# Performance work log

Measured on AMD Instinct MI355X. Metric: run time of the kernel, lower is better.

## Reference

```python
import jax, jax.numpy as jnp
import numpy as np

SCALE = 0.02

def setup_inputs() -> dict:
    key = jax.random.key(0)
    k1, k2 = jax.random.split(key)
    B, D, T, H = 2, 1024, 2048, 16
    x = jax.random.normal(k1, (B, D, T), dtype=jnp.float32)
    qkv = jax.random.normal(k2, (3, H, D, D // H), dtype=jnp.float32) * SCALE
    return {"x": x, "qkv": qkv}

def reference(x, qkv):
    B, D, T = x.shape
    H = qkv.shape[1]
    # fused QKV projection: (B,D,T) x (3,H,D,Dh) -> (3,B,H,T,Dh)
    proj = jnp.einsum('bdt,nhdD->nbhtD', x, qkv)
    q, k, v = proj[0], proj[1], proj[2]
    scale = jnp.sqrt(jnp.asarray(D // H, dtype=x.dtype))
    # scores: (B,H,T,T)
    attn = jax.nn.softmax(jnp.einsum('bhtD,bhTD->bhtT', q, k) / scale, axis=-1)
    # weighted values, head dim placed before time: (B,H,Dh,T)
    out = jnp.einsum('bhtT,bhTD->bhDt', attn, v)
    return out.reshape(B, D, T)
```

## Files before the change

### kernel.cpp

```cpp
#include <hip/hip_runtime.h>

#define B_ 2
#define D_ 1024
#define T_ 2048
#define H_ 16
#define DH_ 64
#define BH_ (B_ * H_)

typedef __attribute__((ext_vector_type(8))) short bf16x8;
typedef __attribute__((ext_vector_type(8))) unsigned short u16x8;
typedef __attribute__((ext_vector_type(4))) float f32x4;

__device__ __forceinline__ unsigned short f2bf(float f) {
    unsigned u = __float_as_uint(f);
    u += 0x7fffu + ((u >> 16) & 1u);
    return (unsigned short)(u >> 16);
}

__global__ __launch_bounds__(256) void xpose_kernel(
    const float* __restrict__ x, unsigned short* __restrict__ xT)
{
    __shared__ __align__(16) unsigned short Ls[64][68];
    const int t0 = blockIdx.x * 64;
    const int d0 = blockIdx.y * 64;
    const int b  = blockIdx.z;
    const int tid = threadIdx.x;

    const float* xb = x + (size_t)b * D_ * T_ + (size_t)d0 * T_ + t0;
    #pragma unroll
    for (int p = 0; p < 4; p++) {
        int i4  = tid + p * 256;
        int row = i4 >> 4;
        int c4  = (i4 & 15) << 2;
        float4 v = *(const float4*)(xb + (size_t)row * T_ + c4);
        ushort4 u;
        u.x = f2bf(v.x); u.y = f2bf(v.y); u.z = f2bf(v.z); u.w = f2bf(v.w);
        *(ushort4*)&Ls[row][c4] = u;
    }
    __syncthreads();
    unsigned short* ob = xT + (size_t)b * T_ * D_ + (size_t)t0 * D_ + d0;
    #pragma unroll
    for (int p = 0; p < 2; p++) {
        int i    = tid + p * 256;
        int orow = i >> 3;
        int oc8  = (i & 7) * 8;
        u16x8 tv;
        #pragma unroll
        for (int j = 0; j < 8; j++) tv[j] = Ls[oc8 + j][orow];
        *(u16x8*)(ob + (size_t)orow * D_ + oc8) = tv;
    }
}

__global__ __launch_bounds__(256) void wpose_kernel(
    const float* __restrict__ w, unsigned short* __restrict__ wT)
{
    __shared__ __align__(16) unsigned short Ls[64][68];
    const int d0 = blockIdx.x * 64;
    const int nh = blockIdx.y;
    const int tid = threadIdx.x;

    const float* wb = w + (size_t)nh * D_ * DH_ + (size_t)d0 * DH_;
    #pragma unroll
    for (int p = 0; p < 4; p++) {
        int i4  = tid + p * 256;
        int row = i4 >> 4;
        int c4  = (i4 & 15) << 2;
        float4 v = *(const float4*)(wb + (size_t)row * DH_ + c4);
        ushort4 u;
        u.x = f2bf(v.x); u.y = f2bf(v.y); u.z = f2bf(v.z); u.w = f2bf(v.w);
        *(ushort4*)&Ls[row][c4] = u;
    }
    __syncthreads();
    unsigned short* ob = wT + (size_t)nh * DH_ * D_ + d0;
    #pragma unroll
    for (int p = 0; p < 2; p++) {
        int i    = tid + p * 256;
        int orow = i >> 3;
        int oc8  = (i & 7) * 8;
        u16x8 tv;
        #pragma unroll
        for (int j = 0; j < 8; j++) tv[j] = Ls[oc8 + j][orow];
        *(u16x8*)(ob + (size_t)orow * D_ + oc8) = tv;
    }
}

#define LX 72

__global__ __launch_bounds__(256) void proj_mfma_kernel(
    const unsigned short* __restrict__ xT, const unsigned short* __restrict__ wT,
    unsigned short* __restrict__ qk, unsigned short* __restrict__ vT)
{
    __shared__ __align__(16) unsigned short Buf[18432];
    unsigned short* Xs = Buf;
    unsigned short* Ws = Buf + 9216;
    unsigned short* Es = Buf;

    const int t0 = blockIdx.x * 128;
    const int y  = blockIdx.y;
    const int n  = y >> 4;
    const int b  = (y >> 3) & 1;
    const int hp = y & 7;

    const unsigned short* xb = xT + (size_t)b * T_ * D_ + (size_t)t0 * D_;
    const unsigned short* wb = wT + (size_t)(n * 16 + 2 * hp) * DH_ * D_;

    const int tid  = threadIdx.x;
    const int wv   = tid >> 6;
    const int lane = tid & 63;
    const int c15  = lane & 15;
    const int quad = lane >> 4;
    const int tq   = (wv & 1) * 64;
    const int dq   = (wv >> 1) * 64;

    f32x4 acc[4][4];
    #pragma unroll
    for (int mt = 0; mt < 4; mt++)
        #pragma unroll
        for (int nt = 0; nt < 4; nt++)
            acc[mt][nt] = (f32x4){0.f, 0.f, 0.f, 0.f};

    for (int k0 = 0; k0 < D_; k0 += 64) {
        __syncthreads();
        #pragma unroll
        for (int p = 0; p < 4; p++) {
            int i    = tid + p * 256;
            int row  = i >> 3;
            int col8 = (i & 7) * 8;
            *(u16x8*)&Xs[row * LX + col8] =
                *(const u16x8*)(xb + (size_t)row * D_ + k0 + col8);
            *(u16x8*)&Ws[row * LX + col8] =
                *(const u16x8*)(wb + (size_t)row * D_ + k0 + col8);
        }
        __syncthreads();

        bf16x8 af[4][2], bf[4][2];
        #pragma unroll
        for (int mt = 0; mt < 4; mt++)
            #pragma unroll
            for (int s = 0; s < 2; s++)
                af[mt][s] = *(bf16x8*)&Xs[(tq + mt * 16 + c15) * LX + quad * 8 + s * 32];
        #pragma unroll
        for (int nt = 0; nt < 4; nt++)
            #pragma unroll
            for (int s = 0; s < 2; s++)
                bf[nt][s] = *(bf16x8*)&Ws[(dq + nt * 16 + c15) * LX + quad * 8 + s * 32];

        #pragma unroll
        for (int mt = 0; mt < 4; mt++)
            #pragma unroll
            for (int nt = 0; nt < 4; nt++)
                #pragma unroll
                for (int s = 0; s < 2; s++)
                    acc[mt][nt] = __builtin_amdgcn_mfma_f32_16x16x32_bf16(
                        af[mt][s], bf[nt][s], acc[mt][nt], 0, 0, 0);
    }

    const float scale = (n == 0) ? 0.125f : 1.0f;
    __syncthreads();
    #pragma unroll
    for (int mt = 0; mt < 4; mt++)
        #pragma unroll
        for (int nt = 0; nt < 4; nt++)
            #pragma unroll
            for (int r = 0; r < 4; r++)
                Es[(tq + mt * 16 + quad * 4 + r) * 136 + dq + nt * 16 + c15] =
                    f2bf(acc[mt][nt][r] * scale);
    __syncthreads();

    if (n < 2) {
        #pragma unroll
        for (int p = 0; p < 8; p++) {
            int i    = tid + p * 256;
            int row  = i >> 4;
            int col8 = (i & 15) * 8;
            int head = col8 >> 6;
            unsigned short* ob = qk +
                ((size_t)(n * 32 + b * 16 + 2 * hp + head) * T_ + t0 + row) * DH_ + (col8 & 63);
            *(u16x8*)ob = *(u16x8*)&Es[row * 136 + col8];
        }
    } else {
        #pragma unroll
        for (int p = 0; p < 8; p++) {
            int i    = tid + p * 256;
            int orow = i >> 4;
            int oc8  = (i & 15) * 8;
            int head = orow >> 6;
            u16x8 tv;
            #pragma unroll
            for (int j = 0; j < 8; j++) tv[j] = Es[(oc8 + j) * 136 + orow];
            unsigned short* ob = vT +
                (size_t)(b * 16 + 2 * hp + head) * DH_ * T_ +
                (size_t)(orow & 63) * T_ + t0 + oc8;
            *(u16x8*)ob = tv;
        }
    }
}

#define LQ 72

__global__ __launch_bounds__(256) void attn_mfma_kernel(
    const unsigned short* __restrict__ qk, const unsigned short* __restrict__ vT,
    float* __restrict__ out)
{
    __shared__ __align__(16) unsigned char smem[37376];
    unsigned short* Ks  = (unsigned short*)smem;
    unsigned short* Vs  = (unsigned short*)(smem + 9216);
    unsigned short* Psb = (unsigned short*)(smem + 18432);
    float*          Os  = (float*)smem;
    float*          Lrow = (float*)(smem + 36864);

    const int t0 = blockIdx.x * 128;
    const int bh = blockIdx.y;

    const unsigned short* qg = qk + ((size_t)bh * T_ + t0) * DH_;
    const unsigned short* kg = qk + ((size_t)(BH_ + bh) * T_) * DH_;
    const unsigned short* vg = vT + (size_t)bh * DH_ * T_;

    const int tid  = threadIdx.x;
    const int wv   = tid >> 6;
    const int lane = tid & 63;
    const int c15  = lane & 15;
    const int quad = lane >> 4;

    unsigned short* Ps = Psb + wv * 2304;

    bf16x8 bq[2][2];
    #pragma unroll
    for (int g = 0; g < 2; g++)
        #pragma unroll
        for (int s = 0; s < 2; s++)
            bq[g][s] = *(const bf16x8*)(qg +
                (size_t)(wv * 32 + g * 16 + c15) * DH_ + quad * 8 + s * 32);

    float lsum[2] = {0.f, 0.f};
    f32x4 Oacc[2][4];
    #pragma unroll
    for (int g = 0; g < 2; g++)
        #pragma unroll
        for (int nt = 0; nt < 4; nt++)
            Oacc[g][nt] = (f32x4){0.f, 0.f, 0.f, 0.f};

    for (int tau = 0; tau < T_; tau += 64) {
        __syncthreads();
        #pragma unroll
        for (int p = 0; p < 2; p++) {
            int i    = tid + p * 256;
            int row  = i >> 3;
            int col8 = (i & 7) * 8;
            *(u16x8*)&Ks[row * LQ + col8] =
                *(const u16x8*)(kg + (size_t)(tau + row) * DH_ + col8);
            *(u16x8*)&Vs[row * LQ + col8] =
                *(const u16x8*)(vg + (size_t)row * T_ + tau + col8);
        }
        __syncthreads();

        bf16x8 ak[4][2];
        #pragma unroll
        for (int mt = 0; mt < 4; mt++)
            #pragma unroll
            for (int s = 0; s < 2; s++)
                ak[mt][s] = *(bf16x8*)&Ks[(mt * 16 + c15) * LQ + quad * 8 + s * 32];

        #pragma unroll
        for (int g = 0; g < 2; g++) {
            #pragma unroll
            for (int mt = 0; mt < 4; mt++) {
                f32x4 sa = (f32x4){0.f, 0.f, 0.f, 0.f};
                #pragma unroll
                for (int s = 0; s < 2; s++)
                    sa = __builtin_amdgcn_mfma_f32_16x16x32_bf16(ak[mt][s], bq[g][s], sa, 0, 0, 0);
                float p0 = __expf(sa[0]);
                float p1 = __expf(sa[1]);
                float p2 = __expf(sa[2]);
                float p3 = __expf(sa[3]);
                lsum[g] += (p0 + p1) + (p2 + p3);
                uint2 pk;
                pk.x = (unsigned)f2bf(p0) | ((unsigned)f2bf(p1) << 16);
                pk.y = (unsigned)f2bf(p2) | ((unsigned)f2bf(p3) << 16);
                *(uint2*)&Ps[(g * 16 + c15) * LQ + mt * 16 + quad * 4] = pk;
            }
        }
        __syncthreads();

        bf16x8 bv[4][2];
        #pragma unroll
        for (int nt = 0; nt < 4; nt++)
            #pragma unroll
            for (int s = 0; s < 2; s++)
                bv[nt][s] = *(bf16x8*)&Vs[(nt * 16 + c15) * LQ + quad * 8 + s * 32];
        #pragma unroll
        for (int g = 0; g < 2; g++)
            #pragma unroll
            for (int s = 0; s < 2; s++) {
                bf16x8 ap = *(bf16x8*)&Ps[(g * 16 + c15) * LQ + quad * 8 + s * 32];
                #pragma unroll
                for (int nt = 0; nt < 4; nt++)
                    Oacc[g][nt] = __builtin_amdgcn_mfma_f32_16x16x32_bf16(
                        ap, bv[nt][s], Oacc[g][nt], 0, 0, 0);
            }
    }

    #pragma unroll
    for (int g = 0; g < 2; g++) {
        lsum[g] += __shfl_xor(lsum[g], 16);
        lsum[g] += __shfl_xor(lsum[g], 32);
    }
    if (lane < 16) {
        Lrow[wv * 32 + lane]      = lsum[0];
        Lrow[wv * 32 + 16 + lane] = lsum[1];
    }
    __syncthreads();

    #pragma unroll
    for (int g = 0; g < 2; g++) {
        float linv[4];
        #pragma unroll
        for (int r = 0; r < 4; r++)
            linv[r] = 1.0f / Lrow[wv * 32 + g * 16 + quad * 4 + r];
        #pragma unroll
        for (int nt = 0; nt < 4; nt++)
            #pragma unroll
            for (int r = 0; r < 4; r++)
                Os[(nt * 16 + c15) * 132 + wv * 32 + g * 16 + quad * 4 + r] =
                    Oacc[g][nt][r] * linv[r];
    }
    __syncthreads();

    const int b = bh >> 4, h = bh & 15;
    float* og = out + (size_t)b * D_ * T_ + (size_t)(h * DH_) * T_ + t0;
    #pragma unroll
    for (int p = 0; p < 8; p++) {
        int i   = tid + p * 256;
        int row = i >> 5;
        int c4  = (i & 31) << 2;
        *(float4*)(og + (size_t)row * T_ + c4) = *(float4*)&Os[row * 132 + c4];
    }
}

extern "C" void kernel_launch(void* const* d_in, const int* in_sizes, int n_in,
                              void* d_out, int out_size, void* d_ws, size_t ws_size,
                              hipStream_t stream)
{
    const float* x = (const float*)d_in[0];
    const float* w = (const float*)d_in[1];
    float* out = (float*)d_out;

    unsigned short* qk = (unsigned short*)d_ws;
    unsigned short* vT = (unsigned short*)((char*)d_ws + (24u << 20));
    unsigned short* xT = (unsigned short*)((char*)d_ws + (32u << 20));
    unsigned short* wT = (unsigned short*)((char*)d_ws + (40u << 20));

    xpose_kernel<<<dim3(T_ / 64, D_ / 64, B_), 256, 0, stream>>>(x, xT);
    wpose_kernel<<<dim3(D_ / 64, 3 * H_), 256, 0, stream>>>(w, wT);
    proj_mfma_kernel<<<dim3(T_ / 128, 48), 256, 0, stream>>>(xT, wT, qk, vT);
    attn_mfma_kernel<<<dim3(T_ / 128, BH_), 256, 0, stream>>>(qk, vT, out);
}
```

Before: 203.6 us.

## Make attention waves independent, reading K/V from global memory with XCD-aware block mapping

The attention kernel now gives each wave 16 query rows (64 per block) and has every wave read K and V fragments straight from global memory. This drops the shared-memory K/V staging and the block-wide barriers. Block indices are remapped so the blocks sharing a batch-head land on the same XCD, which should improve L2 reuse of K/V. The trade is more global/L2 traffic and less reuse per block, since each wave reloads the full K/V, and the grid doubles to 1024 blocks.

```diff
diff --git a/kernel.cpp b/kernel.cpp
--- a/kernel.cpp
+++ b/kernel.cpp
@@ -202,15 +202,13 @@
     const unsigned short* __restrict__ qk, const unsigned short* __restrict__ vT,
     float* __restrict__ out)
 {
-    __shared__ __align__(16) unsigned char smem[37376];
-    unsigned short* Ks  = (unsigned short*)smem;
-    unsigned short* Vs  = (unsigned short*)(smem + 9216);
-    unsigned short* Psb = (unsigned short*)(smem + 18432);
-    float*          Os  = (float*)smem;
-    float*          Lrow = (float*)(smem + 36864);
-
-    const int t0 = blockIdx.x * 128;
-    const int bh = blockIdx.y;
+    __shared__ __align__(16) unsigned short Sm[10240];
+
+    const int flat = blockIdx.y * 32 + blockIdx.x;
+    const int xcd  = flat & 7;
+    const int slot = flat >> 3;
+    const int bh   = xcd * 4 + (slot >> 5);
+    const int t0   = (slot & 31) * 64;
 
     const unsigned short* qg = qk + ((size_t)bh * T_ + t0) * DH_;
     const unsigned short* kg = qk + ((size_t)(BH_ + bh) * T_) * DH_;
@@ -222,118 +220,74 @@
     const int c15  = lane & 15;
     const int quad = lane >> 4;
 
-    unsigned short* Ps = Psb + wv * 2304;
-
-    bf16x8 bq[2][2];
-    #pragma unroll
-    for (int g = 0; g < 2; g++)
-        #pragma unroll
-        for (int s = 0; s < 2; s++)
-            bq[g][s] = *(const bf16x8*)(qg +
-                (size_t)(wv * 32 + g * 16 + c15) * DH_ + quad * 8 + s * 32);
-
-    float lsum[2] = {0.f, 0.f};
-    f32x4 Oacc[2][4];
-    #pragma unroll
-    for (int g = 0; g < 2; g++)
-        #pragma unroll
-        for (int nt = 0; nt < 4; nt++)
-            Oacc[g][nt] = (f32x4){0.f, 0.f, 0.f, 0.f};
+    unsigned short* Ps  = Sm + wv * 2560;
+    float*          Osw = (float*)(Sm + wv * 2560);
+
+    bf16x8 bq[2];
+    #pragma unroll
+    for (int s = 0; s < 2; s++)
+        bq[s] = *(const bf16x8*)(qg + (size_t)(wv * 16 + c15) * DH_ + quad * 8 + s * 32);
+
+    float lsum = 0.f;
+    f32x4 Oacc[4];
+    #pragma unroll
+    for (int nt = 0; nt < 4; nt++) Oacc[nt] = (f32x4){0.f, 0.f, 0.f, 0.f};
 
     for (int tau = 0; tau < T_; tau += 64) {
-        __syncthreads();
-        #pragma unroll
-        for (int p = 0; p < 2; p++) {
-            int i    = tid + p * 256;
-            int row  = i >> 3;
-            int col8 = (i & 7) * 8;
-            *(u16x8*)&Ks[row * LQ + col8] =
-                *(const u16x8*)(kg + (size_t)(tau + row) * DH_ + col8);
-            *(u16x8*)&Vs[row * LQ + col8] =
-                *(const u16x8*)(vg + (size_t)row * T_ + tau + col8);
-        }
-        __syncthreads();
-
-        bf16x8 ak[4][2];
-        #pragma unroll
-        for (int mt = 0; mt < 4; mt++)
-            #pragma unroll
-            for (int s = 0; s < 2; s++)
-                ak[mt][s] = *(bf16x8*)&Ks[(mt * 16 + c15) * LQ + quad * 8 + s * 32];
-
-        #pragma unroll
-        for (int g = 0; g < 2; g++) {
-            #pragma unroll
-            for (int mt = 0; mt < 4; mt++) {
-                f32x4 sa = (f32x4){0.f, 0.f, 0.f, 0.f};
-                #pragma unroll
-                for (int s = 0; s < 2; s++)
-                    sa = __builtin_amdgcn_mfma_f32_16x16x32_bf16(ak[mt][s], bq[g][s], sa, 0, 0, 0);
-                float p0 = __expf(sa[0]);
-                float p1 = __expf(sa[1]);
-                float p2 = __expf(sa[2]);
-                float p3 = __expf(sa[3]);
-                lsum[g] += (p0 + p1) + (p2 + p3);
-                uint2 pk;
-                pk.x = (unsigned)f2bf(p0) | ((unsigned)f2bf(p1) << 16);
-                pk.y = (unsigned)f2bf(p2) | ((unsigned)f2bf(p3) << 16);
-                *(uint2*)&Ps[(g * 16 + c15) * LQ + mt * 16 + quad * 4] = pk;
+        #pragma unroll
+        for (int mt = 0; mt < 4; mt++) {
+            f32x4 sa = (f32x4){0.f, 0.f, 0.f, 0.f};
+            #pragma unroll
+            for (int s = 0; s < 2; s++) {
+                bf16x8 ak = *(const bf16x8*)(kg +
+                    (size_t)(tau + mt * 16 + c15) * DH_ + quad * 8 + s * 32);
+                sa = __builtin_amdgcn_mfma_f32_16x16x32_bf16(ak, bq[s], sa, 0, 0, 0);
             }
-        }
-        __syncthreads();
-
-        bf16x8 bv[4][2];
-        #pragma unroll
-        for (int nt = 0; nt < 4; nt++)
-            #pragma unroll
-            for (int s = 0; s < 2; s++)
-                bv[nt][s] = *(bf16x8*)&Vs[(nt * 16 + c15) * LQ + quad * 8 + s * 32];
-        #pragma unroll
-        for (int g = 0; g < 2; g++)
-            #pragma unroll
-            for (int s = 0; s < 2; s++) {
-                bf16x8 ap = *(bf16x8*)&Ps[(g * 16 + c15) * LQ + quad * 8 + s * 32];
-                #pragma unroll
-                for (int nt = 0; nt < 4; nt++)
-                    Oacc[g][nt] = __builtin_amdgcn_mfma_f32_16x16x32_bf16(
-                        ap, bv[nt][s], Oacc[g][nt], 0, 0, 0);
+            float p0 = __expf(sa[0]);
+            float p1 = __expf(sa[1]);
+            float p2 = __expf(sa[2]);
+            float p3 = __expf(sa[3]);
+            lsum += (p0 + p1) + (p2 + p3);
+            uint2 pk;
+            pk.x = (unsigned)f2bf(p0) | ((unsigned)f2bf(p1) << 16);
+            pk.y = (unsigned)f2bf(p2) | ((unsigned)f2bf(p3) << 16);
+            *(uint2*)&Ps[c15 * LQ + mt * 16 + quad * 4] = pk;
+        }
+
+        #pragma unroll
+        for (int s = 0; s < 2; s++) {
+            bf16x8 ap = *(bf16x8*)&Ps[c15 * LQ + quad * 8 + s * 32];
+            #pragma unroll
+            for (int nt = 0; nt < 4; nt++) {
+                bf16x8 bv = *(const bf16x8*)(vg +
+                    (size_t)(nt * 16 + c15) * T_ + tau + quad * 8 + s * 32);
+                Oacc[nt] = __builtin_amdgcn_mfma_f32_16x16x32_bf16(ap, bv, Oacc[nt], 0, 0, 0);
             }
-    }
-
-    #pragma unroll
-    for (int g = 0; g < 2; g++) {
-        lsum[g] += __shfl_xor(lsum[g], 16);
-        lsum[g] += __shfl_xor(lsum[g], 32);
-    }
-    if (lane < 16) {
-        Lrow[wv * 32 + lane]      = lsum[0];
-        Lrow[wv * 32 + 16 + lane] = lsum[1];
-    }
-    __syncthreads();
-
-    #pragma unroll
-    for (int g = 0; g < 2; g++) {
-        float linv[4];
+        }
+    }
+
+    lsum += __shfl_xor(lsum, 16);
+    lsum += __shfl_xor(lsum, 32);
+    float linv[4];
+    #pragma unroll
+    for (int r = 0; r < 4; r++)
+        linv[r] = 1.0f / __shfl(lsum, quad * 4 + r);
+
+    #pragma unroll
+    for (int nt = 0; nt < 4; nt++)
         #pragma unroll
         for (int r = 0; r < 4; r++)
-            linv[r] = 1.0f / Lrow[wv * 32 + g * 16 + quad * 4 + r];
-        #pragma unroll
-        for (int nt = 0; nt < 4; nt++)
-            #pragma unroll
-            for (int r = 0; r < 4; r++)
-                Os[(nt * 16 + c15) * 132 + wv * 32 + g * 16 + quad * 4 + r] =
-                    Oacc[g][nt][r] * linv[r];
-    }
-    __syncthreads();
+            Osw[(nt * 16 + c15) * 20 + quad * 4 + r] = Oacc[nt][r] * linv[r];
 
     const int b = bh >> 4, h = bh & 15;
-    float* og = out + (size_t)b * D_ * T_ + (size_t)(h * DH_) * T_ + t0;
-    #pragma unroll
-    for (int p = 0; p < 8; p++) {
-        int i   = tid + p * 256;
-        int row = i >> 5;
-        int c4  = (i & 31) << 2;
-        *(float4*)(og + (size_t)row * T_ + c4) = *(float4*)&Os[row * 132 + c4];
+    float* og = out + (size_t)b * D_ * T_ + (size_t)(h * DH_) * T_ + t0 + wv * 16;
+    #pragma unroll
+    for (int p = 0; p < 4; p++) {
+        int idx = lane + p * 64;
+        int dh  = idx >> 2;
+        int qs  = (idx & 3) * 4;
+        float4 v = *(float4*)&Osw[dh * 20 + qs];
+        *(float4*)(og + (size_t)dh * T_ + qs) = v;
     }
 }
 
@@ -353,5 +307,5 @@
     xpose_kernel<<<dim3(T_ / 64, D_ / 64, B_), 256, 0, stream>>>(x, xT);
     wpose_kernel<<<dim3(D_ / 64, 3 * H_), 256, 0, stream>>>(w, wT);
     proj_mfma_kernel<<<dim3(T_ / 128, 48), 256, 0, stream>>>(xT, wT, qk, vT);
-    attn_mfma_kernel<<<dim3(T_ / 128, BH_), 256, 0, stream>>>(qk, vT, out);
-}
+    attn_mfma_kernel<<<dim3(32, 32), 256, 0, stream>>>(qk, vT, out);
+}
```

After: 347.4 us. 70.6% more time.

## Register-prefetch global tiles and double-buffer K/V in attention and projection kernels

Applied to the files above, without the earlier changes.

In both MFMA kernels, the next K-slice or K/V tile is loaded into registers before the current one is computed, hiding global memory latency behind the MFMA work. The attention kernel double-buffers K/V in shared memory, XOR-swizzles the P tile to avoid bank conflicts, drops two barriers per iteration, and uses shuffles instead of LDS for the row sums. It also writes output per wave and remaps block indices so heads are spread across the grid. Launch bounds and the projection's LDS padding change too. The extra prefetch registers could lower occupancy.

```diff
diff --git a/kernel.cpp b/kernel.cpp
--- a/kernel.cpp
+++ b/kernel.cpp
@@ -84,15 +84,15 @@
     }
 }
 
-#define LX 72
-
-__global__ __launch_bounds__(256) void proj_mfma_kernel(
+#define LX 80
+
+__global__ __launch_bounds__(256, 3) void proj_mfma_kernel(
     const unsigned short* __restrict__ xT, const unsigned short* __restrict__ wT,
     unsigned short* __restrict__ qk, unsigned short* __restrict__ vT)
 {
-    __shared__ __align__(16) unsigned short Buf[18432];
+    __shared__ __align__(16) unsigned short Buf[20480];
     unsigned short* Xs = Buf;
-    unsigned short* Ws = Buf + 9216;
+    unsigned short* Ws = Buf + 10240;
     unsigned short* Es = Buf;
 
     const int t0 = blockIdx.x * 128;
@@ -112,26 +112,42 @@
     const int tq   = (wv & 1) * 64;
     const int dq   = (wv >> 1) * 64;
 
+    const int srow = tid >> 3;
+    const int scol = (tid & 7) * 8;
+
     f32x4 acc[4][4];
     #pragma unroll
     for (int mt = 0; mt < 4; mt++)
         #pragma unroll
         for (int nt = 0; nt < 4; nt++)
             acc[mt][nt] = (f32x4){0.f, 0.f, 0.f, 0.f};
+
+    u16x8 xreg[4], wreg[4];
+    #pragma unroll
+    for (int p = 0; p < 4; p++) {
+        int row = srow + p * 32;
+        xreg[p] = *(const u16x8*)(xb + (size_t)row * D_ + scol);
+        wreg[p] = *(const u16x8*)(wb + (size_t)row * D_ + scol);
+    }
 
     for (int k0 = 0; k0 < D_; k0 += 64) {
         __syncthreads();
         #pragma unroll
         for (int p = 0; p < 4; p++) {
-            int i    = tid + p * 256;
-            int row  = i >> 3;
-            int col8 = (i & 7) * 8;
-            *(u16x8*)&Xs[row * LX + col8] =
-                *(const u16x8*)(xb + (size_t)row * D_ + k0 + col8);
-            *(u16x8*)&Ws[row * LX + col8] =
-                *(const u16x8*)(wb + (size_t)row * D_ + k0 + col8);
+            int row = srow + p * 32;
+            *(u16x8*)&Xs[row * LX + scol] = xreg[p];
+            *(u16x8*)&Ws[row * LX + scol] = wreg[p];
         }
         __syncthreads();
+
+        if (k0 + 64 < D_) {
+            #pragma unroll
+            for (int p = 0; p < 4; p++) {
+                int row = srow + p * 32;
+                xreg[p] = *(const u16x8*)(xb + (size_t)row * D_ + k0 + 64 + scol);
+                wreg[p] = *(const u16x8*)(wb + (size_t)row * D_ + k0 + 64 + scol);
+            }
+        }
 
         bf16x8 af[4][2], bf[4][2];
         #pragma unroll
@@ -196,21 +212,15 @@
     }
 }
 
-#define LQ 72
-
-__global__ __launch_bounds__(256) void attn_mfma_kernel(
+__global__ __launch_bounds__(256, 2) void attn_mfma_kernel(
     const unsigned short* __restrict__ qk, const unsigned short* __restrict__ vT,
     float* __restrict__ out)
 {
-    __shared__ __align__(16) unsigned char smem[37376];
-    unsigned short* Ks  = (unsigned short*)smem;
-    unsigned short* Vs  = (unsigned short*)(smem + 9216);
-    unsigned short* Psb = (unsigned short*)(smem + 18432);
-    float*          Os  = (float*)smem;
-    float*          Lrow = (float*)(smem + 36864);
-
-    const int t0 = blockIdx.x * 128;
-    const int bh = blockIdx.y;
+    __shared__ __align__(16) unsigned short Sm[24576];
+
+    const int flat = blockIdx.x;
+    const int bh   = (flat & 7) * 4 + ((flat >> 3) >> 4);
+    const int t0   = ((flat >> 3) & 15) * 128;
 
     const unsigned short* qg = qk + ((size_t)bh * T_ + t0) * DH_;
     const unsigned short* kg = qk + ((size_t)(BH_ + bh) * T_) * DH_;
@@ -221,8 +231,12 @@
     const int lane = tid & 63;
     const int c15  = lane & 15;
     const int quad = lane >> 4;
-
-    unsigned short* Ps = Psb + wv * 2304;
+    const int swz  = (c15 & 7) * 8;
+
+    unsigned short* Ps = Sm + 16384 + wv * 2048;
+
+    const int srow = tid >> 3;
+    const int scol = (tid & 7) * 8;
 
     bf16x8 bq[2][2];
     #pragma unroll
@@ -240,26 +254,42 @@
         for (int nt = 0; nt < 4; nt++)
             Oacc[g][nt] = (f32x4){0.f, 0.f, 0.f, 0.f};
 
+    u16x8 kreg[2], vreg[2];
+    #pragma unroll
+    for (int p = 0; p < 2; p++) {
+        int row = srow + p * 32;
+        kreg[p] = *(const u16x8*)(kg + (size_t)row * DH_ + scol);
+        vreg[p] = *(const u16x8*)(vg + (size_t)row * T_ + scol);
+    }
+    #pragma unroll
+    for (int p = 0; p < 2; p++) {
+        int row = srow + p * 32;
+        *(u16x8*)&Sm[row * 64 + scol]        = kreg[p];
+        *(u16x8*)&Sm[4096 + row * 64 + scol] = vreg[p];
+    }
+
     for (int tau = 0; tau < T_; tau += 64) {
+        const int cur = (tau >> 6) & 1;
+        unsigned short* Ks = Sm + cur * 8192;
+        unsigned short* Vs = Ks + 4096;
         __syncthreads();
-        #pragma unroll
-        for (int p = 0; p < 2; p++) {
-            int i    = tid + p * 256;
-            int row  = i >> 3;
-            int col8 = (i & 7) * 8;
-            *(u16x8*)&Ks[row * LQ + col8] =
-                *(const u16x8*)(kg + (size_t)(tau + row) * DH_ + col8);
-            *(u16x8*)&Vs[row * LQ + col8] =
-                *(const u16x8*)(vg + (size_t)row * T_ + tau + col8);
-        }
-        __syncthreads();
+
+        const bool pf = (tau + 64 < T_);
+        if (pf) {
+            #pragma unroll
+            for (int p = 0; p < 2; p++) {
+                int row = srow + p * 32;
+                kreg[p] = *(const u16x8*)(kg + (size_t)(tau + 64 + row) * DH_ + scol);
+                vreg[p] = *(const u16x8*)(vg + (size_t)row * T_ + tau + 64 + scol);
+            }
+        }
 
         bf16x8 ak[4][2];
         #pragma unroll
         for (int mt = 0; mt < 4; mt++)
             #pragma unroll
             for (int s = 0; s < 2; s++)
-                ak[mt][s] = *(bf16x8*)&Ks[(mt * 16 + c15) * LQ + quad * 8 + s * 32];
+                ak[mt][s] = *(bf16x8*)&Ks[(mt * 16 + c15) * 64 + quad * 8 + s * 32];
 
         #pragma unroll
         for (int g = 0; g < 2; g++) {
@@ -277,27 +307,36 @@
                 uint2 pk;
                 pk.x = (unsigned)f2bf(p0) | ((unsigned)f2bf(p1) << 16);
                 pk.y = (unsigned)f2bf(p2) | ((unsigned)f2bf(p3) << 16);
-                *(uint2*)&Ps[(g * 16 + c15) * LQ + mt * 16 + quad * 4] = pk;
-            }
-        }
-        __syncthreads();
+                *(uint2*)&Ps[(g * 16 + c15) * 64 + ((mt * 16 + quad * 4) ^ swz)] = pk;
+            }
+        }
 
         bf16x8 bv[4][2];
         #pragma unroll
         for (int nt = 0; nt < 4; nt++)
             #pragma unroll
             for (int s = 0; s < 2; s++)
-                bv[nt][s] = *(bf16x8*)&Vs[(nt * 16 + c15) * LQ + quad * 8 + s * 32];
+                bv[nt][s] = *(bf16x8*)&Vs[(nt * 16 + c15) * 64 + quad * 8 + s * 32];
         #pragma unroll
         for (int g = 0; g < 2; g++)
             #pragma unroll
             for (int s = 0; s < 2; s++) {
-                bf16x8 ap = *(bf16x8*)&Ps[(g * 16 + c15) * LQ + quad * 8 + s * 32];
+                bf16x8 ap = *(bf16x8*)&Ps[(g * 16 + c15) * 64 + ((quad * 8 + s * 32) ^ swz)];
                 #pragma unroll
                 for (int nt = 0; nt < 4; nt++)
                     Oacc[g][nt] = __builtin_amdgcn_mfma_f32_16x16x32_bf16(
                         ap, bv[nt][s], Oacc[g][nt], 0, 0, 0);
             }
+
+        if (pf) {
+            unsigned short* Kn = Sm + (1 - cur) * 8192;
+            #pragma unroll
+            for (int p = 0; p < 2; p++) {
+                int row = srow + p * 32;
+                *(u16x8*)&Kn[row * 64 + scol]        = kreg[p];
+                *(u16x8*)&Kn[4096 + row * 64 + scol] = vreg[p];
+            }
+        }
     }
 
     #pragma unroll
@@ -305,35 +344,33 @@
         lsum[g] += __shfl_xor(lsum[g], 16);
         lsum[g] += __shfl_xor(lsum[g], 32);
     }
-    if (lane < 16) {
-        Lrow[wv * 32 + lane]      = lsum[0];
-        Lrow[wv * 32 + 16 + lane] = lsum[1];
-    }
-    __syncthreads();
-
-    #pragma unroll
-    for (int g = 0; g < 2; g++) {
-        float linv[4];
+    float linv[2][4];
+    #pragma unroll
+    for (int g = 0; g < 2; g++)
         #pragma unroll
         for (int r = 0; r < 4; r++)
-            linv[r] = 1.0f / Lrow[wv * 32 + g * 16 + quad * 4 + r];
+            linv[g][r] = 1.0f / __shfl(lsum[g], quad * 4 + r);
+
+    __syncthreads();
+    float* Osw = (float*)(void*)Sm + wv * 2304;
+    #pragma unroll
+    for (int g = 0; g < 2; g++)
         #pragma unroll
         for (int nt = 0; nt < 4; nt++)
             #pragma unroll
             for (int r = 0; r < 4; r++)
-                Os[(nt * 16 + c15) * 132 + wv * 32 + g * 16 + quad * 4 + r] =
-                    Oacc[g][nt][r] * linv[r];
-    }
-    __syncthreads();
+                Osw[(nt * 16 + c15) * 36 + g * 16 + quad * 4 + r] =
+                    Oacc[g][nt][r] * linv[g][r];
 
     const int b = bh >> 4, h = bh & 15;
-    float* og = out + (size_t)b * D_ * T_ + (size_t)(h * DH_) * T_ + t0;
+    float* og = out + (size_t)b * D_ * T_ + (size_t)(h * DH_) * T_ + t0 + wv * 32;
     #pragma unroll
     for (int p = 0; p < 8; p++) {
-        int i   = tid + p * 256;
-        int row = i >> 5;
-        int c4  = (i & 31) << 2;
-        *(float4*)(og + (size_t)row * T_ + c4) = *(float4*)&Os[row * 132 + c4];
+        int idx = lane + p * 64;
+        int dh  = idx >> 3;
+        int qs  = (idx & 7) * 4;
+        float4 v = *(float4*)&Osw[dh * 36 + qs];
+        *(float4*)(og + (size_t)dh * T_ + qs) = v;
     }
 }
 
@@ -353,5 +390,5 @@
     xpose_kernel<<<dim3(T_ / 64, D_ / 64, B_), 256, 0, stream>>>(x, xT);
     wpose_kernel<<<dim3(D_ / 64, 3 * H_), 256, 0, stream>>>(w, wT);
     proj_mfma_kernel<<<dim3(T_ / 128, 48), 256, 0, stream>>>(xT, wT, qk, vT);
-    attn_mfma_kernel<<<dim3(T_ / 128, BH_), 256, 0, stream>>>(qk, vT, out);
-}
+    attn_mfma_kernel<<<512, 256, 0, stream>>>(qk, vT, out);
+}
```

After: 175.8 us. 13.7% less time.
